# Kernel optimization log

Hardware: AMD Instinct MI355X
Metric: run time of the kernel (lower is better)

## Reference

```python
import jax, jax.numpy as jnp
import numpy as np

H = 1024      # hidden_size
NH = 16       # attention heads
DH = H // NH  # head dim
B, S = 4, 2048
EPS = 1e-12


def setup_inputs() -> dict:
    key = jax.random.key(0)
    ks = jax.random.split(key, 9)
    sc = 1.0 / np.sqrt(H)
    inp = {
        "input_tensor": jax.random.normal(ks[0], (B, S, H), dtype=jnp.float32),
        "Wq": jax.random.normal(ks[1], (H, H), dtype=jnp.float32) * sc,
        "bq": jnp.zeros((H,), jnp.float32),
        "Wk": jax.random.normal(ks[2], (H, H), dtype=jnp.float32) * sc,
        "bk": jnp.zeros((H,), jnp.float32),
        "Wv": jax.random.normal(ks[3], (H, H), dtype=jnp.float32) * sc,
        "bv": jnp.zeros((H,), jnp.float32),
        "Wo": jax.random.normal(ks[4], (H, H), dtype=jnp.float32) * sc,
        "bo": jnp.zeros((H,), jnp.float32),
        "gamma": jnp.ones((H,), jnp.float32),
        "beta": jnp.zeros((H,), jnp.float32),
    }
    return inp


def _heads(x):
    # [B,S,H] -> [B,NH,S,DH]
    b, s, _ = x.shape
    return x.reshape(b, s, NH, DH).transpose(0, 2, 1, 3)


def reference(input_tensor, Wq, bq, Wk, bk, Wv, bv, Wo, bo, gamma, beta):
    q = _heads(input_tensor @ Wq.T + bq)
    k = _heads(input_tensor @ Wk.T + bk)
    v = _heads(input_tensor @ Wv.T + bv)
    scores = jnp.einsum("bhqd,bhkd->bhqk", q, k) / jnp.sqrt(jnp.float32(DH))
    probs = jax.nn.softmax(scores, axis=-1)  # dropout p=0 -> identity
    ctx = jnp.einsum("bhqk,bhkd->bhqd", probs, v)
    ctx = ctx.transpose(0, 2, 1, 3).reshape(input_tensor.shape)  # [B,S,H]
    h = ctx @ Wo.T + bo
    x = h + input_tensor
    u = jnp.mean(x, axis=-1, keepdims=True)
    s2 = jnp.mean((x - u) ** 2, axis=-1, keepdims=True)
    xn = (x - u) / jnp.sqrt(s2 + EPS)
    return gamma * xn + beta
```

## Files before the change

### kernel.cpp

```cpp
#include <hip/hip_runtime.h>
#include <math.h>

#define H   1024
#define NH  16
#define DH  64
#define BB  4
#define SS  2048
#define M_ROWS (BB*SS)
#define EPS 1e-12f
#define QSCALE 0.18033688011112042f

typedef __attribute__((ext_vector_type(4))) float f32x4;
typedef __attribute__((ext_vector_type(8))) short bf16x8;
typedef const __attribute__((address_space(1))) void* as1cvp;
typedef __attribute__((address_space(3))) void*       as3vp;
typedef const __attribute__((address_space(1))) ushort* as1u;
typedef __attribute__((address_space(3))) ushort*       as3u;

__device__ __forceinline__ unsigned short f2bf(float f) {
    union { float f; unsigned u; } x; x.f = f;
    unsigned r = x.u + 0x7fffu + ((x.u >> 16) & 1u);
    return (unsigned short)(r >> 16);
}
__device__ __forceinline__ unsigned pk2bf(float lo, float hi) {
    return __builtin_amdgcn_perm(__float_as_uint(hi), __float_as_uint(lo), 0x07060302u);
}

__global__ __launch_bounds__(256)
void cvt_all(const float4* __restrict__ x,
             const float4* __restrict__ wq, const float4* __restrict__ wk,
             const float4* __restrict__ wv, const float4* __restrict__ wo,
             ushort4* __restrict__ xb, ushort4* __restrict__ wqb,
             ushort4* __restrict__ wkb, ushort4* __restrict__ wvb,
             ushort4* __restrict__ wob)
{
    int id = blockIdx.x * 256 + threadIdx.x;
    const float4* src; ushort4* dst; int off;
    if (id < 2097152) { src = x; dst = xb; off = id; }
    else {
        int t = id - 2097152, wsel = t >> 18;
        off = t & 262143;
        src = wsel == 0 ? wq : wsel == 1 ? wk : wsel == 2 ? wv : wo;
        dst = wsel == 0 ? wqb : wsel == 1 ? wkb : wsel == 2 ? wvb : wob;
    }
    float4 v = src[off];
    ushort4 o; o.x = f2bf(v.x); o.y = f2bf(v.y); o.z = f2bf(v.z); o.w = f2bf(v.w);
    dst[off] = o;
}

__device__ __forceinline__ void gemm_core_128(const ushort* __restrict__ A,
                                              const ushort* __restrict__ Wt,
                                              ushort* AsP, ushort* BsP,
                                              int row0, int col0, int K,
                                              f32x4 (&acc)[4][4])
{
    const int tid = threadIdx.x, lane = tid & 63, w = tid >> 6;
    const int wr = w >> 1, wc = w & 1, l15 = lane & 15, quad = lane >> 4;
    const int lr = lane >> 2, kc = lane & 3;
    const int qs  = kc ^ ((lr >> 1) & 3);
    const int qsw = (quad ^ ((l15 >> 1) & 3)) * 8;

    const as1u gA = (as1u)A;
    const as1u gB = (as1u)Wt;
    as3u lA = (as3u)AsP;
    as3u lB = (as3u)BsP;

    const int ra = (w * 2) * 16 + lr;
    const int rb = ra + 16;

    for (int k0 = 0; k0 < K; k0 += 32) {
        __builtin_amdgcn_global_load_lds((as1cvp)(gA + (size_t)(row0 + ra) * K + k0 + qs * 8),
                                         (as3vp)(lA + (w * 2 + 0) * 512), 16, 0, 0);
        __builtin_amdgcn_global_load_lds((as1cvp)(gA + (size_t)(row0 + rb) * K + k0 + qs * 8),
                                         (as3vp)(lA + (w * 2 + 1) * 512), 16, 0, 0);
        __builtin_amdgcn_global_load_lds((as1cvp)(gB + (size_t)(col0 + ra) * K + k0 + qs * 8),
                                         (as3vp)(lB + (w * 2 + 0) * 512), 16, 0, 0);
        __builtin_amdgcn_global_load_lds((as1cvp)(gB + (size_t)(col0 + rb) * K + k0 + qs * 8),
                                         (as3vp)(lB + (w * 2 + 1) * 512), 16, 0, 0);
        __syncthreads();
        bf16x8 af[4], bfr[4];
        #pragma unroll
        for (int rt = 0; rt < 4; ++rt)
            af[rt] = *(const bf16x8*)&AsP[(wr * 64 + rt * 16 + l15) * 32 + qsw];
        #pragma unroll
        for (int ct = 0; ct < 4; ++ct)
            bfr[ct] = *(const bf16x8*)&BsP[(wc * 64 + ct * 16 + l15) * 32 + qsw];
        #pragma unroll
        for (int rt = 0; rt < 4; ++rt)
            #pragma unroll
            for (int ct = 0; ct < 4; ++ct)
                acc[rt][ct] = __builtin_amdgcn_mfma_f32_16x16x32_bf16(af[rt], bfr[ct], acc[rt][ct], 0, 0, 0);
        __syncthreads();
    }
}

__global__ __launch_bounds__(256)
void qkv_gemm(const ushort* __restrict__ xb,
              const ushort* __restrict__ Wqb, const ushort* __restrict__ Wkb,
              const ushort* __restrict__ Wvb,
              const float* __restrict__ bq, const float* __restrict__ bk,
              const float* __restrict__ bv,
              ushort* __restrict__ Qb, ushort* __restrict__ Kb, ushort* __restrict__ Vt)
{
    __shared__ ushort As[128 * 32];
    __shared__ ushort Bs[128 * 32];
    const int z = blockIdx.z;
    const ushort* Wt  = z == 0 ? Wqb : z == 1 ? Wkb : Wvb;
    const float* bias = z == 0 ? bq  : z == 1 ? bk  : bv;
    const int row0 = blockIdx.y * 128, col0 = blockIdx.x * 128;

    f32x4 acc[4][4];
    #pragma unroll
    for (int i = 0; i < 4; ++i)
        #pragma unroll
        for (int j = 0; j < 4; ++j)
            acc[i][j] = (f32x4){0.f, 0.f, 0.f, 0.f};

    gemm_core_128(xb, Wt, As, Bs, row0, col0, H, acc);

    const int tid = threadIdx.x, lane = tid & 63, w = tid >> 6;
    const int wr = w >> 1, wc = w & 1, l15 = lane & 15, quad = lane >> 4;

    #pragma unroll
    for (int rt = 0; rt < 4; ++rt) {
        const int r0g = row0 + wr * 64 + rt * 16 + quad * 4;
        #pragma unroll
        for (int ct = 0; ct < 4; ++ct) {
            const int c = col0 + wc * 64 + ct * 16 + l15;
            const float bs = bias[c];
            if (z == 0) {
                #pragma unroll
                for (int i = 0; i < 4; ++i)
                    Qb[(size_t)(r0g + i) * H + c] = f2bf((acc[rt][ct][i] + bs) * QSCALE);
            } else if (z == 1) {
                #pragma unroll
                for (int i = 0; i < 4; ++i)
                    Kb[(size_t)(r0g + i) * H + c] = f2bf(acc[rt][ct][i] + bs);
            } else {
                const int bb = r0g >> 11, s0 = r0g & 2047;
                const int hh = c >> 6, dd = c & 63;
                ushort4 o;
                o.x = f2bf(acc[rt][ct][0] + bs);
                o.y = f2bf(acc[rt][ct][1] + bs);
                o.z = f2bf(acc[rt][ct][2] + bs);
                o.w = f2bf(acc[rt][ct][3] + bs);
                *(ushort4*)&Vt[(((size_t)(bb * 16 + hh) * 64 + dd) << 11) + s0] = o;
            }
        }
    }
}

__global__ __launch_bounds__(256)
void oproj_gemm(const ushort* __restrict__ ctxb, const ushort* __restrict__ Wob,
                const float* __restrict__ bo, const float* __restrict__ res,
                float* __restrict__ Xr)
{
    __shared__ ushort As[128 * 32];
    __shared__ ushort Bs[128 * 32];
    const int row0 = blockIdx.y * 128, col0 = blockIdx.x * 128;

    f32x4 acc[4][4];
    #pragma unroll
    for (int i = 0; i < 4; ++i)
        #pragma unroll
        for (int j = 0; j < 4; ++j)
            acc[i][j] = (f32x4){0.f, 0.f, 0.f, 0.f};

    gemm_core_128(ctxb, Wob, As, Bs, row0, col0, H, acc);

    const int tid = threadIdx.x, lane = tid & 63, w = tid >> 6;
    const int wr = w >> 1, wc = w & 1, l15 = lane & 15, quad = lane >> 4;

    #pragma unroll
    for (int rt = 0; rt < 4; ++rt) {
        const int r0g = row0 + wr * 64 + rt * 16 + quad * 4;
        #pragma unroll
        for (int ct = 0; ct < 4; ++ct) {
            const int c = col0 + wc * 64 + ct * 16 + l15;
            const float bs = bo[c];
            #pragma unroll
            for (int i = 0; i < 4; ++i) {
                size_t idx = (size_t)(r0g + i) * H + c;
                Xr[idx] = acc[rt][ct][i] + bs + res[idx];
            }
        }
    }
}

#define KTILE 64
#define NKT (SS / KTILE)

__global__ __launch_bounds__(256, 3)
void flash_attn_mfma(const ushort* __restrict__ Qb, const ushort* __restrict__ Kb,
                     const ushort* __restrict__ Vt, ushort* __restrict__ ctx)
{
    __shared__ __align__(16) ushort Ks[2][KTILE * 64];
    __shared__ __align__(16) ushort Vs[2][64 * KTILE];

    const int tid  = threadIdx.x;
    const int lane = tid & 63;
    const int w    = tid >> 6;
    const int l15  = lane & 15, quad = lane >> 4;
    const int bh   = blockIdx.x & 63;
    const int qt   = blockIdx.x >> 6;
    const int b    = bh >> 4, h = bh & 15;
    const int row0 = qt * 128 + w * 32;
    const size_t qk_base = (size_t)(b * SS) * H + h * DH;
    const size_t vt_base = (size_t)((b * 16 + h) * 64) * SS;

    const as1u gK = (const as1u)Kb;
    const as1u gV = (const as1u)Vt;

    const int srow = lane >> 3;
    const int c8   = lane & 7;
    const int sck0 = c8 ^ ((srow & 3) | (((w * 2 + 0) & 1) << 2));
    const int sck1 = c8 ^ ((srow & 3) | (((w * 2 + 1) & 1) << 2));

    const int fL = (l15 & 3) | (((l15 >> 2) & 1) << 2);
    const int fV = (l15 & 3) | (((l15 >> 3) & 1) << 2);
    const int rA = 8 * (l15 >> 2) + (l15 & 3);
    int kOff0[4], kOff1[4], vOff0[4], vOff1[4];
    #pragma unroll
    for (int ct = 0; ct < 4; ++ct) {
        const int r = rA + (ct & 1) * 4 + (ct >> 1) * 32;
        kOff0[ct] = r * 64 + ((quad ^ fL) * 8);
        kOff1[ct] = r * 64 + (((4 | quad) ^ fL) * 8);
    }
    #pragma unroll
    for (int dt = 0; dt < 4; ++dt) {
        const int rv = dt * 16 + l15;
        vOff0[dt] = rv * 64 + ((quad ^ fV) * 8);
        vOff1[dt] = rv * 64 + (((4 | quad) ^ fV) * 8);
    }

    bf16x8 aq[2][2];
    #pragma unroll
    for (int g = 0; g < 2; ++g) {
        const size_t qrow = qk_base + (size_t)(row0 + g * 16 + l15) * H;
        aq[g][0] = *(const bf16x8*)&Qb[qrow + quad * 8];
        aq[g][1] = *(const bf16x8*)&Qb[qrow + 32 + quad * 8];
    }

    union { unsigned u[4]; bf16x8 v; } ONES;
    #pragma unroll
    for (int i = 0; i < 4; ++i) ONES.u[i] = 0x3F803F80u;

    f32x4 acc_l[2];
    f32x4 o[2][4];
    #pragma unroll
    for (int g = 0; g < 2; ++g) {
        acc_l[g] = (f32x4){0.f, 0.f, 0.f, 0.f};
        #pragma unroll
        for (int dt = 0; dt < 4; ++dt) o[g][dt] = (f32x4){0.f, 0.f, 0.f, 0.f};
    }

    const as1u gK0 = gK + qk_base + (size_t)(w * 16 + srow) * H;
    const as1u gV0 = gV + vt_base + (size_t)(w * 16 + srow) * SS;

    __builtin_amdgcn_global_load_lds((as1cvp)(gK0 + sck0 * 8),
                                     (as3vp)(&Ks[0][(w * 16) * 64]), 16, 0, 0);
    __builtin_amdgcn_global_load_lds((as1cvp)(gK0 + (size_t)8 * H + sck1 * 8),
                                     (as3vp)(&Ks[0][(w * 16 + 8) * 64]), 16, 0, 0);
    __builtin_amdgcn_global_load_lds((as1cvp)(gV0 + sck0 * 8),
                                     (as3vp)(&Vs[0][(w * 16) * 64]), 16, 0, 0);
    __builtin_amdgcn_global_load_lds((as1cvp)(gV0 + (size_t)8 * SS + sck1 * 8),
                                     (as3vp)(&Vs[0][(w * 16 + 8) * 64]), 16, 0, 0);

    for (int kt = 0; kt < NKT; ++kt) {
        __syncthreads();

        if (kt + 1 < NKT) {
            const int j0 = (kt + 1) * KTILE;
            const int nb = (kt + 1) & 1;
            __builtin_amdgcn_global_load_lds((as1cvp)(gK0 + (size_t)j0 * H + sck0 * 8),
                                             (as3vp)(&Ks[nb][(w * 16) * 64]), 16, 0, 0);
            __builtin_amdgcn_global_load_lds((as1cvp)(gK0 + (size_t)(j0 + 8) * H + sck1 * 8),
                                             (as3vp)(&Ks[nb][(w * 16 + 8) * 64]), 16, 0, 0);
            __builtin_amdgcn_global_load_lds((as1cvp)(gV0 + j0 + sck0 * 8),
                                             (as3vp)(&Vs[nb][(w * 16) * 64]), 16, 0, 0);
            __builtin_amdgcn_global_load_lds((as1cvp)(gV0 + (size_t)8 * SS + j0 + sck1 * 8),
                                             (as3vp)(&Vs[nb][(w * 16 + 8) * 64]), 16, 0, 0);
        }

        const ushort* Ktile = Ks[kt & 1];
        const ushort* Vtile = Vs[kt & 1];

        f32x4 s[2][4];
        __builtin_amdgcn_s_setprio(1);
        #pragma unroll
        for (int ct = 0; ct < 4; ++ct) {
            const bf16x8 k0 = *(const bf16x8*)&Ktile[kOff0[ct]];
            const bf16x8 k1 = *(const bf16x8*)&Ktile[kOff1[ct]];
            #pragma unroll
            for (int g = 0; g < 2; ++g) {
                f32x4 z = (f32x4){0.f, 0.f, 0.f, 0.f};
                z = __builtin_amdgcn_mfma_f32_16x16x32_bf16(k0, aq[g][0], z, 0, 0, 0);
                z = __builtin_amdgcn_mfma_f32_16x16x32_bf16(k1, aq[g][1], z, 0, 0, 0);
                s[g][ct] = z;
            }
        }
        __builtin_amdgcn_s_setprio(0);

        union { unsigned u[4]; bf16x8 v; } A[2][2];
        #pragma unroll
        for (int g = 0; g < 2; ++g) {
            #pragma unroll
            for (int ct = 0; ct < 4; ++ct) {
                const float p0 = __builtin_amdgcn_exp2f(s[g][ct][0]);
                const float p1 = __builtin_amdgcn_exp2f(s[g][ct][1]);
                const float p2 = __builtin_amdgcn_exp2f(s[g][ct][2]);
                const float p3 = __builtin_amdgcn_exp2f(s[g][ct][3]);
                A[g][ct >> 1].u[(ct & 1) * 2 + 0] = pk2bf(p0, p1);
                A[g][ct >> 1].u[(ct & 1) * 2 + 1] = pk2bf(p2, p3);
            }
        }

        __builtin_amdgcn_s_setprio(1);
        #pragma unroll
        for (int g = 0; g < 2; ++g) {
            acc_l[g] = __builtin_amdgcn_mfma_f32_16x16x32_bf16(A[g][0].v, ONES.v, acc_l[g], 0, 0, 0);
            acc_l[g] = __builtin_amdgcn_mfma_f32_16x16x32_bf16(A[g][1].v, ONES.v, acc_l[g], 0, 0, 0);
        }
        #pragma unroll
        for (int dt = 0; dt < 4; ++dt) {
            const bf16x8 v0 = *(const bf16x8*)&Vtile[vOff0[dt]];
            const bf16x8 v1 = *(const bf16x8*)&Vtile[vOff1[dt]];
            #pragma unroll
            for (int g = 0; g < 2; ++g) {
                o[g][dt] = __builtin_amdgcn_mfma_f32_16x16x32_bf16(A[g][0].v, v0, o[g][dt], 0, 0, 0);
                o[g][dt] = __builtin_amdgcn_mfma_f32_16x16x32_bf16(A[g][1].v, v1, o[g][dt], 0, 0, 0);
            }
        }
        __builtin_amdgcn_s_setprio(0);
    }

    #pragma unroll
    for (int g = 0; g < 2; ++g) {
        #pragma unroll
        for (int i = 0; i < 4; ++i) {
            const float inv = 1.f / acc_l[g][i];
            const int r = row0 + g * 16 + quad * 4 + i;
            #pragma unroll
            for (int dt = 0; dt < 4; ++dt)
                ctx[qk_base + (size_t)r * H + dt * 16 + l15] = f2bf(o[g][dt][i] * inv);
        }
    }
}

__global__ __launch_bounds__(256)
void ln_kernel(const float* __restrict__ Xr, const float* __restrict__ gamma,
               const float* __restrict__ beta, float* __restrict__ out)
{
    __shared__ float red[256], red2[256];
    const int row = blockIdx.x;
    const int tid = threadIdx.x;
    const float4 v = ((const float4*)(Xr + (size_t)row * H))[tid];
    float s  = v.x + v.y + v.z + v.w;
    float ss = v.x * v.x + v.y * v.y + v.z * v.z + v.w * v.w;
    red[tid] = s; red2[tid] = ss;
    __syncthreads();
    for (int st = 128; st > 0; st >>= 1) {
        if (tid < st) { red[tid] += red[tid + st]; red2[tid] += red2[tid + st]; }
        __syncthreads();
    }
    const float mean = red[0] * (1.f / H);
    const float var  = red2[0] * (1.f / H) - mean * mean;
    const float rstd = rsqrtf(var + EPS);
    const float4 g  = ((const float4*)gamma)[tid];
    const float4 be = ((const float4*)beta)[tid];
    float4 o;
    o.x = g.x * (v.x - mean) * rstd + be.x;
    o.y = g.y * (v.y - mean) * rstd + be.y;
    o.z = g.z * (v.z - mean) * rstd + be.z;
    o.w = g.w * (v.w - mean) * rstd + be.w;
    ((float4*)(out + (size_t)row * H))[tid] = o;
}

extern "C" void kernel_launch(void* const* d_in, const int* in_sizes, int n_in,
                              void* d_out, int out_size, void* d_ws, size_t ws_size,
                              hipStream_t stream)
{
    const float* x     = (const float*)d_in[0];
    const float* Wq    = (const float*)d_in[1];
    const float* bq    = (const float*)d_in[2];
    const float* Wk    = (const float*)d_in[3];
    const float* bk    = (const float*)d_in[4];
    const float* Wv    = (const float*)d_in[5];
    const float* bv    = (const float*)d_in[6];
    const float* Wo    = (const float*)d_in[7];
    const float* bo    = (const float*)d_in[8];
    const float* gamma = (const float*)d_in[9];
    const float* beta  = (const float*)d_in[10];

    char* ws = (char*)d_ws;
    ushort* xb  = (ushort*)(ws);
    ushort* Wqb = (ushort*)(ws + (size_t)(16 << 20));
    ushort* Wkb = (ushort*)(ws + (size_t)(18 << 20));
    ushort* Wvb = (ushort*)(ws + (size_t)(20 << 20));
    ushort* Wob = (ushort*)(ws + (size_t)(22 << 20));
    ushort* Qb  = (ushort*)(ws + (size_t)(24 << 20));
    ushort* Kb  = (ushort*)(ws + (size_t)(40 << 20));
    ushort* Vt  = (ushort*)(ws + (size_t)(56 << 20));
    float*  Xr  = (float*) (ws + (size_t)(40 << 20));

    cvt_all<<<12288, 256, 0, stream>>>((const float4*)x, (const float4*)Wq, (const float4*)Wk,
                                       (const float4*)Wv, (const float4*)Wo,
                                       (ushort4*)xb, (ushort4*)Wqb, (ushort4*)Wkb,
                                       (ushort4*)Wvb, (ushort4*)Wob);

    qkv_gemm<<<dim3(H / 128, M_ROWS / 128, 3), 256, 0, stream>>>(
        xb, Wqb, Wkb, Wvb, bq, bk, bv, Qb, Kb, Vt);

    flash_attn_mfma<<<BB * NH * (SS / 128), 256, 0, stream>>>(Qb, Kb, Vt, Qb );

    oproj_gemm<<<dim3(H / 128, M_ROWS / 128), 256, 0, stream>>>(Qb, Wob, bo, x, Xr);

    ln_kernel<<<M_ROWS, 256, 0, stream>>>(Xr, gamma, beta, (float*)d_out);
}
```

Baseline: 287.7 us.

## Double-buffer GEMM LDS tiles with prefetch and use wave-shuffle LayerNorm reduction

```diff
diff --git a/kernel.cpp b/kernel.cpp
--- a/kernel.cpp
+++ b/kernel.cpp
@@ -50,7 +50,7 @@
 
 __device__ __forceinline__ void gemm_core_128(const ushort* __restrict__ A,
                                               const ushort* __restrict__ Wt,
-                                              ushort* AsP, ushort* BsP,
+                                              ushort* ldsP,
                                               int row0, int col0, int K,
                                               f32x4 (&acc)[4][4])
 {
@@ -62,22 +62,38 @@
 
     const as1u gA = (as1u)A;
     const as1u gB = (as1u)Wt;
-    as3u lA = (as3u)AsP;
-    as3u lB = (as3u)BsP;
+    as3u lds = (as3u)ldsP;
 
     const int ra = (w * 2) * 16 + lr;
     const int rb = ra + 16;
-
+    const size_t gAr0 = (size_t)(row0 + ra) * K + qs * 8;
+    const size_t gAr1 = (size_t)(row0 + rb) * K + qs * 8;
+    const size_t gBr0 = (size_t)(col0 + ra) * K + qs * 8;
+    const size_t gBr1 = (size_t)(col0 + rb) * K + qs * 8;
+    const int dA0 = (w * 2 + 0) * 512;
+    const int dA1 = (w * 2 + 1) * 512;
+
+    __builtin_amdgcn_global_load_lds((as1cvp)(gA + gAr0), (as3vp)(lds + dA0), 16, 0, 0);
+    __builtin_amdgcn_global_load_lds((as1cvp)(gA + gAr1), (as3vp)(lds + dA1), 16, 0, 0);
+    __builtin_amdgcn_global_load_lds((as1cvp)(gB + gBr0), (as3vp)(lds + 4096 + dA0), 16, 0, 0);
+    __builtin_amdgcn_global_load_lds((as1cvp)(gB + gBr1), (as3vp)(lds + 4096 + dA1), 16, 0, 0);
+
+    int bofs = 0;
     for (int k0 = 0; k0 < K; k0 += 32) {
-        __builtin_amdgcn_global_load_lds((as1cvp)(gA + (size_t)(row0 + ra) * K + k0 + qs * 8),
-                                         (as3vp)(lA + (w * 2 + 0) * 512), 16, 0, 0);
-        __builtin_amdgcn_global_load_lds((as1cvp)(gA + (size_t)(row0 + rb) * K + k0 + qs * 8),
-                                         (as3vp)(lA + (w * 2 + 1) * 512), 16, 0, 0);
-        __builtin_amdgcn_global_load_lds((as1cvp)(gB + (size_t)(col0 + ra) * K + k0 + qs * 8),
-                                         (as3vp)(lB + (w * 2 + 0) * 512), 16, 0, 0);
-        __builtin_amdgcn_global_load_lds((as1cvp)(gB + (size_t)(col0 + rb) * K + k0 + qs * 8),
-                                         (as3vp)(lB + (w * 2 + 1) * 512), 16, 0, 0);
         __syncthreads();
+        const int nofs = bofs ^ 8192;
+        if (k0 + 32 < K) {
+            __builtin_amdgcn_global_load_lds((as1cvp)(gA + gAr0 + k0 + 32),
+                                             (as3vp)(lds + nofs + dA0), 16, 0, 0);
+            __builtin_amdgcn_global_load_lds((as1cvp)(gA + gAr1 + k0 + 32),
+                                             (as3vp)(lds + nofs + dA1), 16, 0, 0);
+            __builtin_amdgcn_global_load_lds((as1cvp)(gB + gBr0 + k0 + 32),
+                                             (as3vp)(lds + nofs + 4096 + dA0), 16, 0, 0);
+            __builtin_amdgcn_global_load_lds((as1cvp)(gB + gBr1 + k0 + 32),
+                                             (as3vp)(lds + nofs + 4096 + dA1), 16, 0, 0);
+        }
+        const ushort* AsP = ldsP + bofs;
+        const ushort* BsP = ldsP + bofs + 4096;
         bf16x8 af[4], bfr[4];
         #pragma unroll
         for (int rt = 0; rt < 4; ++rt)
@@ -90,11 +106,11 @@
             #pragma unroll
             for (int ct = 0; ct < 4; ++ct)
                 acc[rt][ct] = __builtin_amdgcn_mfma_f32_16x16x32_bf16(af[rt], bfr[ct], acc[rt][ct], 0, 0, 0);
-        __syncthreads();
-    }
-}
-
-__global__ __launch_bounds__(256)
+        bofs = nofs;
+    }
+}
+
+__global__ __launch_bounds__(256, 3)
 void qkv_gemm(const ushort* __restrict__ xb,
               const ushort* __restrict__ Wqb, const ushort* __restrict__ Wkb,
               const ushort* __restrict__ Wvb,
@@ -102,8 +118,7 @@
               const float* __restrict__ bv,
               ushort* __restrict__ Qb, ushort* __restrict__ Kb, ushort* __restrict__ Vt)
 {
-    __shared__ ushort As[128 * 32];
-    __shared__ ushort Bs[128 * 32];
+    __shared__ __align__(16) ushort Ls[4 * 4096];
     const int z = blockIdx.z;
     const ushort* Wt  = z == 0 ? Wqb : z == 1 ? Wkb : Wvb;
     const float* bias = z == 0 ? bq  : z == 1 ? bk  : bv;
@@ -116,7 +131,7 @@
         for (int j = 0; j < 4; ++j)
             acc[i][j] = (f32x4){0.f, 0.f, 0.f, 0.f};
 
-    gemm_core_128(xb, Wt, As, Bs, row0, col0, H, acc);
+    gemm_core_128(xb, Wt, Ls, row0, col0, H, acc);
 
     const int tid = threadIdx.x, lane = tid & 63, w = tid >> 6;
     const int wr = w >> 1, wc = w & 1, l15 = lane & 15, quad = lane >> 4;
@@ -150,13 +165,12 @@
     }
 }
 
-__global__ __launch_bounds__(256)
+__global__ __launch_bounds__(256, 3)
 void oproj_gemm(const ushort* __restrict__ ctxb, const ushort* __restrict__ Wob,
                 const float* __restrict__ bo, const float* __restrict__ res,
                 float* __restrict__ Xr)
 {
-    __shared__ ushort As[128 * 32];
-    __shared__ ushort Bs[128 * 32];
+    __shared__ __align__(16) ushort Ls[4 * 4096];
     const int row0 = blockIdx.y * 128, col0 = blockIdx.x * 128;
 
     f32x4 acc[4][4];
@@ -166,7 +180,7 @@
         for (int j = 0; j < 4; ++j)
             acc[i][j] = (f32x4){0.f, 0.f, 0.f, 0.f};
 
-    gemm_core_128(ctxb, Wob, As, Bs, row0, col0, H, acc);
+    gemm_core_128(ctxb, Wob, Ls, row0, col0, H, acc);
 
     const int tid = threadIdx.x, lane = tid & 63, w = tid >> 6;
     const int wr = w >> 1, wc = w & 1, l15 = lane & 15, quad = lane >> 4;
@@ -351,20 +365,24 @@
 void ln_kernel(const float* __restrict__ Xr, const float* __restrict__ gamma,
                const float* __restrict__ beta, float* __restrict__ out)
 {
-    __shared__ float red[256], red2[256];
+    __shared__ float red[4], red2[4];
     const int row = blockIdx.x;
     const int tid = threadIdx.x;
+    const int lane = tid & 63, w = tid >> 6;
     const float4 v = ((const float4*)(Xr + (size_t)row * H))[tid];
     float s  = v.x + v.y + v.z + v.w;
     float ss = v.x * v.x + v.y * v.y + v.z * v.z + v.w * v.w;
-    red[tid] = s; red2[tid] = ss;
+    #pragma unroll
+    for (int d = 1; d < 64; d <<= 1) {
+        s  += __shfl_xor(s, d);
+        ss += __shfl_xor(ss, d);
+    }
+    if (lane == 0) { red[w] = s; red2[w] = ss; }
     __syncthreads();
-    for (int st = 128; st > 0; st >>= 1) {
-        if (tid < st) { red[tid] += red[tid + st]; red2[tid] += red2[tid + st]; }
-        __syncthreads();
-    }
-    const float mean = red[0] * (1.f / H);
-    const float var  = red2[0] * (1.f / H) - mean * mean;
+    s  = red[0]  + red[1]  + red[2]  + red[3];
+    ss = red2[0] + red2[1] + red2[2] + red2[3];
+    const float mean = s * (1.f / H);
+    const float var  = ss * (1.f / H) - mean * mean;
     const float rstd = rsqrtf(var + EPS);
     const float4 g  = ((const float4*)gamma)[tid];
     const float4 be = ((const float4*)beta)[tid];
```

After: 298.2 us. +3.7%, slower.
